# Performance work log

Measured on AMD Instinct MI355X. Metric: run time of the kernel, lower is better.

The kernel has to match this reference:

```python
import jax, jax.numpy as jnp
import numpy as np

N, M, RANK = 1024, 4096, 32


def setup_inputs() -> dict:
    key = jax.random.key(0)
    kW, kH, kT = jax.random.split(key, 3)
    W = jax.random.uniform(kW, (N, RANK), dtype=jnp.float32)
    H = jax.random.uniform(kH, (RANK, M), dtype=jnp.float32)
    tau = jax.random.uniform(kT, (N, RANK), dtype=jnp.float32) * 2.0 - 1.0
    return {"W": W, "H": H, "tau": tau}


def reference(W, H, tau):
    # Hf: FFT along last axis of softplus(H) -> (rank, M) complex64
    Hf = jnp.fft.fft(jax.nn.softplus(H), axis=-1)
    m = H.shape[-1]
    f = (jnp.arange(m, dtype=jnp.float32) / m)  # (M,)
    # phase ramp: omega[n,d,m] = exp(-i*2*pi*tau[n,d]*f[m])
    phase = tau[:, :, None] * f[None, None, :]          # (N, rank, M) float32
    omega = jnp.exp((-2j * jnp.pi) * phase)             # complex64
    spW = jax.nn.softplus(W)                            # (N, rank)
    # V[n,m] = sum_d spW[n,d] * omega[n,d,m] * Hf[d,m]
    V = jnp.einsum('nd,ndm,dm->nm', spW.astype(omega.dtype), omega, Hf)
    return V
```

## Files before the change

### kernel.cpp

```cpp
#include <hip/hip_runtime.h>
#include <hip/hip_bf16.h>
#include <math.h>

#ifndef M_PI
#define M_PI 3.14159265358979323846
#endif

constexpr int N    = 1024;
constexpr int M    = 4096;
constexpr int RANK = 32;
constexpr float PHI1 = -1.5339807878856412e-3f;

typedef __attribute__((ext_vector_type(8))) short bf16x8;
typedef __attribute__((ext_vector_type(4))) float f32x4;

__device__ __forceinline__ float softplus_f(float x) {
    const float t = __expf(-fabsf(x));
    return fmaxf(x, 0.0f) + __logf(1.0f + t);
}

__device__ __forceinline__ unsigned pack_bf16x2(float a, float b) {
    __hip_bfloat162 p;
    p.x = __float2bfloat16(a);
    p.y = __float2bfloat16(b);
    unsigned r;
    __builtin_memcpy(&r, &p, 4);
    return r;
}

__global__ __launch_bounds__(256) void dft_s1(const float* __restrict__ H,
                                              float* __restrict__ GR,
                                              float* __restrict__ GI) {
    __shared__ float sh[M];
    const int d = blockIdx.y, tid = threadIdx.x;
    const float4* H4 = (const float4*)(H + d * M);
    for (int i = tid; i < M / 4; i += 256) {
        const float4 v = H4[i];
        ((float4*)sh)[i] = make_float4(softplus_f(v.x), softplus_f(v.y),
                                       softplus_f(v.z), softplus_f(v.w));
    }
    __syncthreads();

    const int k0 = tid & 63;
    const int r0 = blockIdx.x * 8 + (tid >> 6) * 2;
    float twR0 = 1.f, twI0 = 0.f, aR0 = 0.f, aI0 = 0.f;
    float twR1 = 1.f, twI1 = 0.f, aR1 = 0.f, aI1 = 0.f;
    float s0, c0, s1, c1;
    __sincosf((-2.0f * (float)M_PI / 64.0f) * (float)r0,       &s0, &c0);
    __sincosf((-2.0f * (float)M_PI / 64.0f) * (float)(r0 + 1), &s1, &c1);

    for (int k1 = 0; k1 < 64; ++k1) {
        const float h = sh[(k1 << 6) + k0];
        aR0 = fmaf(h, twR0, aR0);  aI0 = fmaf(h, twI0, aI0);
        aR1 = fmaf(h, twR1, aR1);  aI1 = fmaf(h, twI1, aI1);
        float nR = fmaf(twR0, c0, -twI0 * s0);
        float nI = fmaf(twR0, s0,  twI0 * c0);
        twR0 = nR; twI0 = nI;
        nR = fmaf(twR1, c1, -twI1 * s1);
        nI = fmaf(twR1, s1,  twI1 * c1);
        twR1 = nR; twI1 = nI;
    }
    const int base = d * 4096 + r0 * 64 + k0;
    GR[base]      = aR0;  GI[base]      = aI0;
    GR[base + 64] = aR1;  GI[base + 64] = aI1;
}

__global__ __launch_bounds__(256) void dft_s2(const float* __restrict__ GR,
                                              const float* __restrict__ GI,
                                              float* __restrict__ HfR,
                                              float* __restrict__ HfI) {
    __shared__ float sGR[64 * 65], sGI[64 * 65];
    const int d = blockIdx.y, tid = threadIdx.x;
    const float4* gr4 = (const float4*)(GR + d * 4096);
    const float4* gi4 = (const float4*)(GI + d * 4096);
    for (int i4 = tid; i4 < 1024; i4 += 256) {
        const int r = i4 >> 4, k0 = (i4 & 15) << 2;
        const float4 vr = gr4[i4];
        const float4 vi = gi4[i4];
        const int p = r * 65 + k0;
        sGR[p] = vr.x; sGR[p+1] = vr.y; sGR[p+2] = vr.z; sGR[p+3] = vr.w;
        sGI[p] = vi.x; sGI[p+1] = vi.y; sGI[p+2] = vi.z; sGI[p+3] = vi.w;
    }
    __syncthreads();

    const int m = blockIdx.x * 256 + tid;
    const int rb = (m & 63) * 65;
    float ss, sc; __sincosf(PHI1 * (float)m, &ss, &sc);
    float tR_ = 1.f, tI_ = 0.f, accR = 0.f, accI = 0.f;
    #pragma unroll 8
    for (int k0 = 0; k0 < 64; ++k0) {
        const float gr = sGR[rb + k0], gi = sGI[rb + k0];
        accR = fmaf(tR_, gr, fmaf(-tI_, gi, accR));
        accI = fmaf(tR_, gi, fmaf( tI_, gr, accI));
        const float nR = fmaf(tR_, sc, -tI_ * ss);
        const float nI = fmaf(tR_, ss,  tI_ * sc);
        tR_ = nR; tI_ = nI;
    }
    HfR[d * M + m] = accR;
    HfI[d * M + m] = accI;
}

__device__ __forceinline__ void a_terms(float w, float t, float mcF, float* o) {
    const float sw = softplus_f(w);
    const float a1 = PHI1 * t;
    float s0, c0; __sincosf(a1 * mcF, &s0, &c0);
    const float R0 = sw * c0,  I0 = sw * s0;
    const float R1 = -a1 * I0, I1 = a1 * R0;
    const float h  = 0.5f * a1;
    const float R2 = -h * I1,  I2 = h * R1;
    o[0] = R0; o[1] = -I0; o[2] = R1; o[3] = -I1; o[4] = R2; o[5] = -I2;
}

__global__ __launch_bounds__(256, 4) void einsum_mfma(const float* __restrict__ W,
                                                      const float* __restrict__ tau,
                                                      const float* __restrict__ HfR,
                                                      const float* __restrict__ HfI,
                                                      float* __restrict__ out_f) {
    __shared__ __attribute__((aligned(16))) unsigned short sB[6][64][40];
    const int tid   = threadIdx.x;
    const int mBase = blockIdx.x * 64;
    const int nBase = blockIdx.y * 64;

    const int wv = tid >> 6, lane = tid & 63;
    const int q = lane >> 4, l = lane & 15;
    const int nA = nBase + wv * 16 + l;
    const int d8 = q << 3;
    const float mcF = (float)(mBase + 32);

    const float4 w0 = *(const float4*)(W   + nA * RANK + d8);
    const float4 w1 = *(const float4*)(W   + nA * RANK + d8 + 4);
    const float4 t0 = *(const float4*)(tau + nA * RANK + d8);
    const float4 t1 = *(const float4*)(tau + nA * RANK + d8 + 4);

    for (int e = tid; e < 512; e += 256) {
        const int mloc = e & 63;
        const int d0   = (e >> 6) << 2;
        const float dlt = (float)mloc - 32.0f;
        const float dq  = dlt * dlt;
        const float* pR = HfR + d0 * M + mBase + mloc;
        const float* pI = HfI + d0 * M + mBase + mloc;
        float r0 = pR[0], r1 = pR[M], r2 = pR[2*M], r3 = pR[3*M];
        float i0 = pI[0], i1 = pI[M], i2 = pI[2*M], i3 = pI[3*M];

        uint2 v;
        v.x = pack_bf16x2(r0, r1);           v.y = pack_bf16x2(r2, r3);
        *(uint2*)&sB[0][mloc][d0] = v;
        v.x = pack_bf16x2(i0, i1);           v.y = pack_bf16x2(i2, i3);
        *(uint2*)&sB[1][mloc][d0] = v;
        v.x = pack_bf16x2(r0*dlt, r1*dlt);   v.y = pack_bf16x2(r2*dlt, r3*dlt);
        *(uint2*)&sB[2][mloc][d0] = v;
        v.x = pack_bf16x2(i0*dlt, i1*dlt);   v.y = pack_bf16x2(i2*dlt, i3*dlt);
        *(uint2*)&sB[3][mloc][d0] = v;
        v.x = pack_bf16x2(r0*dq, r1*dq);     v.y = pack_bf16x2(r2*dq, r3*dq);
        *(uint2*)&sB[4][mloc][d0] = v;
        v.x = pack_bf16x2(i0*dq, i1*dq);     v.y = pack_bf16x2(i2*dq, i3*dq);
        *(uint2*)&sB[5][mloc][d0] = v;
    }

    const float wj[8] = {w0.x,w0.y,w0.z,w0.w,w1.x,w1.y,w1.z,w1.w};
    const float tj[8] = {t0.x,t0.y,t0.z,t0.w,t1.x,t1.y,t1.z,t1.w};
    unsigned uA[6][4];
    #pragma unroll
    for (int p = 0; p < 4; ++p) {
        float f0[6], f1[6];
        a_terms(wj[2*p],   tj[2*p],   mcF, f0);
        a_terms(wj[2*p+1], tj[2*p+1], mcF, f1);
        #pragma unroll
        for (int k = 0; k < 6; ++k) uA[k][p] = pack_bf16x2(f0[k], f1[k]);
    }
    bf16x8 fA[6];
    #pragma unroll
    for (int k = 0; k < 6; ++k) __builtin_memcpy(&fA[k], uA[k], 16);
    __syncthreads();

    for (int mt = 0; mt < 4; ++mt) {
        const int mL = (mt << 4) + l;
        const bf16x8 b0 = *(const bf16x8*)&sB[0][mL][d8];
        const bf16x8 b1 = *(const bf16x8*)&sB[1][mL][d8];
        const bf16x8 b2 = *(const bf16x8*)&sB[2][mL][d8];
        const bf16x8 b3 = *(const bf16x8*)&sB[3][mL][d8];
        const bf16x8 b4 = *(const bf16x8*)&sB[4][mL][d8];
        const bf16x8 b5 = *(const bf16x8*)&sB[5][mL][d8];

        f32x4 acc = {0.f, 0.f, 0.f, 0.f};
        acc = __builtin_amdgcn_mfma_f32_16x16x32_bf16(fA[0], b0, acc, 0, 0, 0);
        acc = __builtin_amdgcn_mfma_f32_16x16x32_bf16(fA[1], b1, acc, 0, 0, 0);
        acc = __builtin_amdgcn_mfma_f32_16x16x32_bf16(fA[2], b2, acc, 0, 0, 0);
        acc = __builtin_amdgcn_mfma_f32_16x16x32_bf16(fA[3], b3, acc, 0, 0, 0);
        acc = __builtin_amdgcn_mfma_f32_16x16x32_bf16(fA[4], b4, acc, 0, 0, 0);
        acc = __builtin_amdgcn_mfma_f32_16x16x32_bf16(fA[5], b5, acc, 0, 0, 0);

        #pragma unroll
        for (int r = 0; r < 4; ++r)
            out_f[(size_t)(nBase + wv * 16 + (q << 2) + r) * M
                  + mBase + (mt << 4) + l] = acc[r];
    }
}

__global__ __launch_bounds__(256) void dft_fused(const float* __restrict__ H,
                                                 float* __restrict__ HfR,
                                                 float* __restrict__ HfI) {
    __shared__ float  sh[M];
    __shared__ float2 sG[64 * 65];
    const int d = blockIdx.y, tid = threadIdx.x;
    for (int k = tid; k < M; k += 256) sh[k] = softplus_f(H[d * M + k]);
    __syncthreads();

    const int k0 = tid & 63;
    const int rB = (tid >> 6) * 16;
    float twR[16], twI[16], stR[16], stI[16], aR[16], aI[16];
    #pragma unroll
    for (int rr = 0; rr < 16; ++rr) {
        const float ang = (-2.0f * (float)M_PI / 64.0f) * (float)(rB + rr);
        __sincosf(ang, &stI[rr], &stR[rr]);
        twR[rr] = 1.f; twI[rr] = 0.f; aR[rr] = 0.f; aI[rr] = 0.f;
    }
    for (int k1 = 0; k1 < 64; ++k1) {
        const float h = sh[(k1 << 6) + k0];
        #pragma unroll
        for (int rr = 0; rr < 16; ++rr) {
            aR[rr] = fmaf(h, twR[rr], aR[rr]);
            aI[rr] = fmaf(h, twI[rr], aI[rr]);
            const float nR = fmaf(twR[rr], stR[rr], -twI[rr] * stI[rr]);
            const float nI = fmaf(twR[rr], stI[rr],  twI[rr] * stR[rr]);
            twR[rr] = nR; twI[rr] = nI;
        }
    }
    #pragma unroll
    for (int rr = 0; rr < 16; ++rr)
        sG[k0 * 65 + rB + rr] = make_float2(aR[rr], aI[rr]);
    __syncthreads();

    const int mBase = blockIdx.x * 1024;
    for (int j = 0; j < 4; ++j) {
        const int m = mBase + j * 256 + tid;
        const int r = m & 63;
        float ss, sc; __sincosf(PHI1 * (float)m, &ss, &sc);
        float tR_ = 1.f, tI_ = 0.f, accR = 0.f, accI = 0.f;
        #pragma unroll 8
        for (int qq = 0; qq < 64; ++qq) {
            const float2 g = sG[qq * 65 + r];
            accR = fmaf(tR_, g.x, fmaf(-tI_, g.y, accR));
            accI = fmaf(tR_, g.y, fmaf( tI_, g.x, accI));
            const float nR = fmaf(tR_, sc, -tI_ * ss);
            const float nI = fmaf(tR_, ss,  tI_ * sc);
            tR_ = nR; tI_ = nI;
        }
        HfR[d * M + m] = accR;
        HfI[d * M + m] = accI;
    }
}

template <bool CPLX, int U>
__global__ __launch_bounds__(256) void einsum_kernel(const float* __restrict__ W,
                                                     const float* __restrict__ tau,
                                                     const float* __restrict__ HfR,
                                                     const float* __restrict__ HfI,
                                                     float* __restrict__ out_f) {
    constexpr int ROWS = 16 * U;
    constexpr int MT   = 128;
    __shared__ float2 sHf[16 * MT];
    __shared__ float  sW[ROWS][RANK], sT[ROWS][RANK];
    const int tid   = threadIdx.x;
    const int mBase = blockIdx.x * MT;
    const int nBase = blockIdx.y * ROWS;

    for (int i = tid; i < ROWS * RANK; i += 256) {
        const int n_ = i >> 5, dd = i & 31;
        sW[n_][dd] = softplus_f(W[(nBase + n_) * RANK + dd]);
        sT[n_][dd] = tau[(nBase + n_) * RANK + dd];
    }

    const int nl = tid >> 4, chunk = tid & 15;
    const int m0 = mBase + (chunk << 3);

    float accR[U][8], accI[U][8];
    #pragma unroll
    for (int u = 0; u < U; ++u)
        #pragma unroll
        for (int j = 0; j < 8; ++j) { accR[u][j] = 0.f; if (CPLX) accI[u][j] = 0.f; }

    for (int half = 0; half < 2; ++half) {
        __syncthreads();
        for (int e = tid; e < 16 * 64; e += 256) {
            const int dl = e >> 6, p = e & 63;
            const int mm = p << 1;
            const int base = (half * 16 + dl) * M + mBase + mm;
            const float2 r2 = *(const float2*)(HfR + base);
            const float2 q2 = *(const float2*)(HfI + base);
            const int c = mm >> 3, j0 = mm & 7;
            float2* s2 = sHf + (dl << 7);
            s2[(j0 << 4) + c]       = make_float2(r2.x, q2.x);
            s2[((j0 + 1) << 4) + c] = make_float2(r2.y, q2.y);
        }
        __syncthreads();

        #pragma unroll 1
        for (int dl = 0; dl < 16; ++dl) {
            const int dd = (half << 4) + dl;
            float aR_[U], aI_[U], bR_[U], bI_[U], K[U];
            #pragma unroll
            for (int u = 0; u < U; ++u) {
                const float t = sT[nl * U + u][dd], w = sW[nl * U + u][dd];
                const float a1 = PHI1 * t;
                float sp, cp; __sincosf(a1, &sp, &cp);
                float s0, c0; __sincosf(a1 * (float)m0, &s0, &c0);
                aR_[u] = w * c0;
                aI_[u] = w * s0;
                bR_[u] = fmaf(aR_[u], cp, -aI_[u] * sp);
                bI_[u] = fmaf(aI_[u], cp,  aR_[u] * sp);
                K[u]   = 2.0f * cp;
            }
            int idx = (dl << 7) + chunk;
            #pragma unroll
            for (int j = 0; j < 8; ++j) {
                const float2 h = sHf[idx];
                #pragma unroll
                for (int u = 0; u < U; ++u) {
                    accR[u][j] = fmaf(aR_[u], h.x, fmaf(-aI_[u], h.y, accR[u][j]));
                    if (CPLX) accI[u][j] = fmaf(aR_[u], h.y, fmaf(aI_[u], h.x, accI[u][j]));
                    const float nR = fmaf(K[u], bR_[u], -aR_[u]);
                    const float nI = fmaf(K[u], bI_[u], -aI_[u]);
                    aR_[u] = bR_[u]; aI_[u] = bI_[u];
                    bR_[u] = nR;     bI_[u] = nI;
                }
                idx += 16;
            }
        }
    }

    #pragma unroll
    for (int u = 0; u < U; ++u) {
        const int n = nBase + nl * U + u;
        if (CPLX) {
            float2* o2 = ((float2*)out_f) + (size_t)n * M + m0;
            #pragma unroll
            for (int qq = 0; qq < 4; ++qq)
                ((float4*)o2)[qq] = make_float4(accR[u][2*qq], accI[u][2*qq],
                                                accR[u][2*qq+1], accI[u][2*qq+1]);
        } else {
            float* op = out_f + (size_t)n * M + m0;
            ((float4*)op)[0] = make_float4(accR[u][0], accR[u][1], accR[u][2], accR[u][3]);
            ((float4*)op)[1] = make_float4(accR[u][4], accR[u][5], accR[u][6], accR[u][7]);
        }
    }
}

__global__ __launch_bounds__(256) void tail_real(const float* __restrict__ W,
                                                 const float* __restrict__ tau,
                                                 const float* __restrict__ stashR,
                                                 const float* __restrict__ stashI,
                                                 float* __restrict__ out_f) {
    __shared__ float stR[32 * 32], stI[32 * 32];
    __shared__ float sW[64][RANK], sT[64][RANK];
    const int tid = threadIdx.x;
    const int c0  = blockIdx.x * 32;
    const int nBase = N - 64;
    for (int i = tid; i < 64 * RANK; i += 256) {
        const int n_ = i >> 5, dd = i & 31;
        sW[n_][dd] = softplus_f(W[(nBase + n_) * RANK + dd]);
        sT[n_][dd] = tau[(nBase + n_) * RANK + dd];
    }
    for (int i = tid; i < 32 * 32; i += 256) {
        const int d_ = i >> 5, mm = i & 31;
        stR[i] = stashR[d_ * M + c0 + mm];
        stI[i] = stashI[d_ * M + c0 + mm];
    }
    __syncthreads();
    const int n = tid >> 2, chunk = tid & 3;
    const int m0 = c0 + chunk;
    float acc[8];
    #pragma unroll
    for (int j = 0; j < 8; ++j) acc[j] = 0.f;
    for (int d = 0; d < RANK; ++d) {
        const float t = sT[n][d], w = sW[n][d];
        const float a1 = PHI1 * t;
        float ss, sc; __sincosf(a1 * 4.0f, &ss, &sc);
        float s0, c0f; __sincosf(a1 * (float)m0, &s0, &c0f);
        float tR_ = w * c0f, tI_ = w * s0;
        int idx = (d << 5) + chunk;
        #pragma unroll
        for (int j = 0; j < 8; ++j) {
            acc[j] = fmaf(tR_, stR[idx], fmaf(-tI_, stI[idx], acc[j]));
            const float nR = fmaf(tR_, sc, -tI_ * ss);
            const float nI = fmaf(tR_, ss,  tI_ * sc);
            tR_ = nR; tI_ = nI;
            idx += 4;
        }
    }
    #pragma unroll
    for (int j = 0; j < 8; ++j)
        out_f[(size_t)(nBase + n) * M + m0 + (j << 2)] = acc[j];
}

__global__ __launch_bounds__(256) void tail_cplx(const float* __restrict__ W,
                                                 const float* __restrict__ tau,
                                                 const float* __restrict__ stashR,
                                                 const float* __restrict__ stashI,
                                                 float* __restrict__ out_f) {
    const int nBase = N - 32;
    __shared__ float sW[32][RANK], sT[32][RANK];
    const int tid = threadIdx.x, mBase = blockIdx.x * 256;
    for (int i = tid; i < 32 * RANK; i += 256) {
        const int n_ = i >> 5, dd = i & 31;
        sW[n_][dd] = softplus_f(W[(nBase + n_) * RANK + dd]);
        sT[n_][dd] = tau[(nBase + n_) * RANK + dd];
    }
    const int m = mBase + tid;
    float hr[RANK], hi[RANK];
    #pragma unroll
    for (int d = 0; d < RANK; ++d) { hr[d] = stashR[d * M + m]; hi[d] = stashI[d * M + m]; }
    __syncthreads();
    const float phi = PHI1 * (float)m;
    for (int n_ = 0; n_ < 32; ++n_) {
        float aR = 0.f, aI = 0.f;
        #pragma unroll
        for (int d = 0; d < RANK; ++d) {
            const float t = sT[n_][d], w = sW[n_][d];
            float s, c; __sincosf(t * phi, &s, &c);
            const float cw = c * w, sw = s * w;
            aR = fmaf(cw, hr[d], fmaf(-sw, hi[d], aR));
            aI = fmaf(cw, hi[d], fmaf( sw, hr[d], aI));
        }
        ((float2*)out_f)[(size_t)(nBase + n_) * M + m] = make_float2(aR, aI);
    }
}

extern "C" void kernel_launch(void* const* d_in, const int* in_sizes, int n_in,
                              void* d_out, int out_size, void* d_ws, size_t ws_size,
                              hipStream_t stream) {
    const float* W   = (const float*)d_in[0];
    const float* H   = (const float*)d_in[1];
    const float* tau = (const float*)d_in[2];
    float* out_f = (float*)d_out;

    const bool   cplx   = (out_size >= 2 * N * M);
    const size_t planeN = (size_t)RANK * M;

    if (d_ws != nullptr && ws_size >= 4 * planeN * sizeof(float)) {
        float* HfR = (float*)d_ws;
        float* HfI = HfR + planeN;
        float* GR  = HfI + planeN;
        float* GI  = GR  + planeN;
        dft_s1<<<dim3(8, 32), 256, 0, stream>>>(H, GR, GI);
        dft_s2<<<dim3(16, 32), 256, 0, stream>>>(GR, GI, HfR, HfI);
        if (cplx)
            einsum_kernel<true , 2><<<dim3(32, N / 32), 256, 0, stream>>>(W, tau, HfR, HfI, out_f);
        else
            einsum_mfma<<<dim3(64, 16), 256, 0, stream>>>(W, tau, HfR, HfI, out_f);
    } else if (!cplx) {
        float* HfR = out_f + (size_t)(N - 64) * M;
        float* HfI = HfR + planeN;
        dft_fused<<<dim3(4, 32), 256, 0, stream>>>(H, HfR, HfI);
        einsum_kernel<false, 2><<<dim3(32, (N - 64) / 32), 256, 0, stream>>>(W, tau, HfR, HfI, out_f);
        tail_real<<<dim3(128), 256, 0, stream>>>(W, tau, HfR, HfI, out_f);
    } else {
        float* HfR = out_f + 2 * (size_t)N * M - 2 * planeN;
        float* HfI = HfR + planeN;
        dft_fused<<<dim3(4, 32), 256, 0, stream>>>(H, HfR, HfI);
        einsum_kernel<true , 2><<<dim3(32, (N - 32) / 32), 256, 0, stream>>>(W, tau, HfR, HfI, out_f);
        tail_cplx<<<dim3(16), 256, 0, stream>>>(W, tau, HfR, HfI, out_f);
    }
}
```

Before: 82.09 us.

## Fuse DFT stages and MFMA einsum into one cooperative kernel with grid syncs

Replaces the three separate launches (two DFT stages and the MFMA einsum) on the real-output path with a single cooperative kernel of 1024 blocks that separates the phases with grid-wide syncs. The aim is to remove kernel launch gaps and inter-kernel tail effects. The cost is that only 512 blocks work during the DFT phases, and each grid sync adds its own overhead. If the cooperative launch fails, the code falls back to the old three-kernel path.

```diff
diff --git a/kernel.cpp b/kernel.cpp
--- a/kernel.cpp
+++ b/kernel.cpp
@@ -1,10 +1,13 @@
 #include <hip/hip_runtime.h>
+#include <hip/hip_cooperative_groups.h>
 #include <hip/hip_bf16.h>
 #include <math.h>
 
 #ifndef M_PI
 #define M_PI 3.14159265358979323846
 #endif
+
+namespace cg = cooperative_groups;
 
 constexpr int N    = 1024;
 constexpr int M    = 4096;
@@ -26,6 +29,174 @@
     unsigned r;
     __builtin_memcpy(&r, &p, 4);
     return r;
+}
+
+__device__ __forceinline__ void a_terms(float w, float t, float mcF, float* o) {
+    const float sw = softplus_f(w);
+    const float a1 = PHI1 * t;
+    float s0, c0; __sincosf(a1 * mcF, &s0, &c0);
+    const float R0 = sw * c0,  I0 = sw * s0;
+    const float R1 = -a1 * I0, I1 = a1 * R0;
+    const float h  = 0.5f * a1;
+    const float R2 = -h * I1,  I2 = h * R1;
+    o[0] = R0; o[1] = -I0; o[2] = R1; o[3] = -I1; o[4] = R2; o[5] = -I2;
+}
+
+__global__ __launch_bounds__(256, 4) void mega_real(const float* __restrict__ W,
+                                                    const float* __restrict__ tau,
+                                                    const float* __restrict__ H,
+                                                    float* __restrict__ GR,
+                                                    float* __restrict__ GI,
+                                                    float* __restrict__ HfR,
+                                                    float* __restrict__ HfI,
+                                                    float* __restrict__ out_f) {
+    __shared__ __attribute__((aligned(16))) char smem[64 * 65 * 8];
+    const int tid = threadIdx.x;
+    const int bx  = blockIdx.x;
+    cg::grid_group grid = cg::this_grid();
+
+    if (bx < 512) {
+        float* sh = (float*)smem;
+        const int d  = bx >> 4;
+        const int rG = bx & 15;
+        const float4* H4 = (const float4*)(H + d * M);
+        for (int i = tid; i < M / 4; i += 256) {
+            const float4 v = H4[i];
+            ((float4*)sh)[i] = make_float4(softplus_f(v.x), softplus_f(v.y),
+                                           softplus_f(v.z), softplus_f(v.w));
+        }
+        __syncthreads();
+        const int k0 = tid & 63;
+        const int r0 = rG * 4 + (tid >> 6);
+        float s0, c0;
+        __sincosf((-2.0f * (float)M_PI / 64.0f) * (float)r0, &s0, &c0);
+        float twR = 1.f, twI = 0.f, aR = 0.f, aI = 0.f;
+        for (int k1 = 0; k1 < 64; ++k1) {
+            const float h = sh[(k1 << 6) + k0];
+            aR = fmaf(h, twR, aR);  aI = fmaf(h, twI, aI);
+            const float nR = fmaf(twR, c0, -twI * s0);
+            const float nI = fmaf(twR, s0,  twI * c0);
+            twR = nR; twI = nI;
+        }
+        const int base = d * 4096 + r0 * 64 + k0;
+        GR[base] = aR;  GI[base] = aI;
+    }
+    __threadfence();
+    grid.sync();
+
+    if (bx < 512) {
+        float* sGR = (float*)smem;
+        float* sGI = sGR + 64 * 65;
+        const int d  = bx >> 4;
+        const int mG = bx & 15;
+        const float4* gr4 = (const float4*)(GR + d * 4096);
+        const float4* gi4 = (const float4*)(GI + d * 4096);
+        for (int i4 = tid; i4 < 1024; i4 += 256) {
+            const int r = i4 >> 4, k0 = (i4 & 15) << 2;
+            const float4 vr = gr4[i4];
+            const float4 vi = gi4[i4];
+            const int p = r * 65 + k0;
+            sGR[p] = vr.x; sGR[p+1] = vr.y; sGR[p+2] = vr.z; sGR[p+3] = vr.w;
+            sGI[p] = vi.x; sGI[p+1] = vi.y; sGI[p+2] = vi.z; sGI[p+3] = vi.w;
+        }
+        __syncthreads();
+        const int m  = mG * 256 + tid;
+        const int rb = (m & 63) * 65;
+        float ss, sc; __sincosf(PHI1 * (float)m, &ss, &sc);
+        float tR_ = 1.f, tI_ = 0.f, accR = 0.f, accI = 0.f;
+        #pragma unroll 8
+        for (int k0 = 0; k0 < 64; ++k0) {
+            const float gr = sGR[rb + k0], gi = sGI[rb + k0];
+            accR = fmaf(tR_, gr, fmaf(-tI_, gi, accR));
+            accI = fmaf(tR_, gi, fmaf( tI_, gr, accI));
+            const float nR = fmaf(tR_, sc, -tI_ * ss);
+            const float nI = fmaf(tR_, ss,  tI_ * sc);
+            tR_ = nR; tI_ = nI;
+        }
+        HfR[d * M + m] = accR;
+        HfI[d * M + m] = accI;
+    }
+    __threadfence();
+    grid.sync();
+
+    typedef unsigned short (*sBp_t)[64][40];
+    sBp_t sB = (sBp_t)smem;
+    const int mBase = (bx & 63) << 6;
+    const int nBase = (bx >> 6) << 6;
+    const int wv = tid >> 6, lane = tid & 63;
+    const int q = lane >> 4, l = lane & 15;
+    const int nA = nBase + wv * 16 + l;
+    const int d8 = q << 3;
+    const float mcF = (float)(mBase + 32);
+
+    const float4 w0 = *(const float4*)(W   + nA * RANK + d8);
+    const float4 w1 = *(const float4*)(W   + nA * RANK + d8 + 4);
+    const float4 t0 = *(const float4*)(tau + nA * RANK + d8);
+    const float4 t1 = *(const float4*)(tau + nA * RANK + d8 + 4);
+
+    for (int e = tid; e < 512; e += 256) {
+        const int mloc = e & 63;
+        const int d0   = (e >> 6) << 2;
+        const float dlt = (float)mloc - 32.0f;
+        const float dq  = dlt * dlt;
+        const float* pR = HfR + d0 * M + mBase + mloc;
+        const float* pI = HfI + d0 * M + mBase + mloc;
+        float r0 = pR[0], r1 = pR[M], r2 = pR[2*M], r3 = pR[3*M];
+        float i0 = pI[0], i1 = pI[M], i2 = pI[2*M], i3 = pI[3*M];
+
+        uint2 v;
+        v.x = pack_bf16x2(r0, r1);           v.y = pack_bf16x2(r2, r3);
+        *(uint2*)&sB[0][mloc][d0] = v;
+        v.x = pack_bf16x2(i0, i1);           v.y = pack_bf16x2(i2, i3);
+        *(uint2*)&sB[1][mloc][d0] = v;
+        v.x = pack_bf16x2(r0*dlt, r1*dlt);   v.y = pack_bf16x2(r2*dlt, r3*dlt);
+        *(uint2*)&sB[2][mloc][d0] = v;
+        v.x = pack_bf16x2(i0*dlt, i1*dlt);   v.y = pack_bf16x2(i2*dlt, i3*dlt);
+        *(uint2*)&sB[3][mloc][d0] = v;
+        v.x = pack_bf16x2(r0*dq, r1*dq);     v.y = pack_bf16x2(r2*dq, r3*dq);
+        *(uint2*)&sB[4][mloc][d0] = v;
+        v.x = pack_bf16x2(i0*dq, i1*dq);     v.y = pack_bf16x2(i2*dq, i3*dq);
+        *(uint2*)&sB[5][mloc][d0] = v;
+    }
+
+    const float wj[8] = {w0.x,w0.y,w0.z,w0.w,w1.x,w1.y,w1.z,w1.w};
+    const float tj[8] = {t0.x,t0.y,t0.z,t0.w,t1.x,t1.y,t1.z,t1.w};
+    unsigned uA[6][4];
+    #pragma unroll
+    for (int p = 0; p < 4; ++p) {
+        float f0[6], f1[6];
+        a_terms(wj[2*p],   tj[2*p],   mcF, f0);
+        a_terms(wj[2*p+1], tj[2*p+1], mcF, f1);
+        #pragma unroll
+        for (int k = 0; k < 6; ++k) uA[k][p] = pack_bf16x2(f0[k], f1[k]);
+    }
+    bf16x8 fA[6];
+    #pragma unroll
+    for (int k = 0; k < 6; ++k) __builtin_memcpy(&fA[k], uA[k], 16);
+    __syncthreads();
+
+    for (int mt = 0; mt < 4; ++mt) {
+        const int mL = (mt << 4) + l;
+        const bf16x8 b0 = *(const bf16x8*)&sB[0][mL][d8];
+        const bf16x8 b1 = *(const bf16x8*)&sB[1][mL][d8];
+        const bf16x8 b2 = *(const bf16x8*)&sB[2][mL][d8];
+        const bf16x8 b3 = *(const bf16x8*)&sB[3][mL][d8];
+        const bf16x8 b4 = *(const bf16x8*)&sB[4][mL][d8];
+        const bf16x8 b5 = *(const bf16x8*)&sB[5][mL][d8];
+
+        f32x4 acc = {0.f, 0.f, 0.f, 0.f};
+        acc = __builtin_amdgcn_mfma_f32_16x16x32_bf16(fA[0], b0, acc, 0, 0, 0);
+        acc = __builtin_amdgcn_mfma_f32_16x16x32_bf16(fA[1], b1, acc, 0, 0, 0);
+        acc = __builtin_amdgcn_mfma_f32_16x16x32_bf16(fA[2], b2, acc, 0, 0, 0);
+        acc = __builtin_amdgcn_mfma_f32_16x16x32_bf16(fA[3], b3, acc, 0, 0, 0);
+        acc = __builtin_amdgcn_mfma_f32_16x16x32_bf16(fA[4], b4, acc, 0, 0, 0);
+        acc = __builtin_amdgcn_mfma_f32_16x16x32_bf16(fA[5], b5, acc, 0, 0, 0);
+
+        #pragma unroll
+        for (int r = 0; r < 4; ++r)
+            out_f[(size_t)(nBase + wv * 16 + (q << 2) + r) * M
+                  + mBase + (mt << 4) + l] = acc[r];
+    }
 }
 
 __global__ __launch_bounds__(256) void dft_s1(const float* __restrict__ H,
@@ -98,17 +269,6 @@
     }
     HfR[d * M + m] = accR;
     HfI[d * M + m] = accI;
-}
-
-__device__ __forceinline__ void a_terms(float w, float t, float mcF, float* o) {
-    const float sw = softplus_f(w);
-    const float a1 = PHI1 * t;
-    float s0, c0; __sincosf(a1 * mcF, &s0, &c0);
-    const float R0 = sw * c0,  I0 = sw * s0;
-    const float R1 = -a1 * I0, I1 = a1 * R0;
-    const float h  = 0.5f * a1;
-    const float R2 = -h * I1,  I2 = h * R1;
-    o[0] = R0; o[1] = -I0; o[2] = R1; o[3] = -I1; o[4] = R2; o[5] = -I2;
 }
 
 __global__ __launch_bounds__(256, 4) void einsum_mfma(const float* __restrict__ W,
@@ -437,17 +597,34 @@
     const bool   cplx   = (out_size >= 2 * N * M);
     const size_t planeN = (size_t)RANK * M;
 
+    static int coop_ok = -1;
+
     if (d_ws != nullptr && ws_size >= 4 * planeN * sizeof(float)) {
         float* HfR = (float*)d_ws;
         float* HfI = HfR + planeN;
         float* GR  = HfI + planeN;
         float* GI  = GR  + planeN;
-        dft_s1<<<dim3(8, 32), 256, 0, stream>>>(H, GR, GI);
-        dft_s2<<<dim3(16, 32), 256, 0, stream>>>(GR, GI, HfR, HfI);
-        if (cplx)
+
+        if (!cplx) {
+            if (coop_ok != 0) {
+                void* args[8] = {(void*)&W, (void*)&tau, (void*)&H,
+                                 (void*)&GR, (void*)&GI,
+                                 (void*)&HfR, (void*)&HfI, (void*)&out_f};
+                const hipError_t e = hipLaunchCooperativeKernel(
+                    reinterpret_cast<const void*>(mega_real),
+                    dim3(1024), dim3(256), args, 0u, stream);
+                if (e == hipSuccess) { coop_ok = 1; return; }
+                coop_ok = 0;
+                (void)hipGetLastError();
+            }
+            dft_s1<<<dim3(8, 32), 256, 0, stream>>>(H, GR, GI);
+            dft_s2<<<dim3(16, 32), 256, 0, stream>>>(GR, GI, HfR, HfI);
+            einsum_mfma<<<dim3(64, 16), 256, 0, stream>>>(W, tau, HfR, HfI, out_f);
+        } else {
+            dft_s1<<<dim3(8, 32), 256, 0, stream>>>(H, GR, GI);
+            dft_s2<<<dim3(16, 32), 256, 0, stream>>>(GR, GI, HfR, HfI);
             einsum_kernel<true , 2><<<dim3(32, N / 32), 256, 0, stream>>>(W, tau, HfR, HfI, out_f);
-        else
-            einsum_mfma<<<dim3(64, 16), 256, 0, stream>>>(W, tau, HfR, HfI, out_f);
+        }
     } else if (!cplx) {
         float* HfR = out_f + (size_t)(N - 64) * M;
         float* HfI = HfR + planeN;
```

New measurement: 81.58 us. About the same (-0.6%).

## Fuse two-stage DFT into one kernel with residue-class block decomposition

Applied to the files above, without the earlier changes.

Replaces the two DFT kernels, which passed intermediate G arrays through global memory, with one kernel. Each block handles one residue class c of the output frequency modulo 8, computes the 8 first-stage rows it needs into shared memory, then produces the 512 outputs with m ≡ c mod 8. This removes the global round trip for the intermediates and one kernel launch. In exchange, every block recomputes softplus over the full H row (8x redundant loads and softplus work), and the second-stage shared reads come from rows indexed by tid&7, so lanes in a warp read different rows.

```diff
diff --git a/kernel.cpp b/kernel.cpp
--- a/kernel.cpp
+++ b/kernel.cpp
@@ -26,78 +26,6 @@
     unsigned r;
     __builtin_memcpy(&r, &p, 4);
     return r;
-}
-
-__global__ __launch_bounds__(256) void dft_s1(const float* __restrict__ H,
-                                              float* __restrict__ GR,
-                                              float* __restrict__ GI) {
-    __shared__ float sh[M];
-    const int d = blockIdx.y, tid = threadIdx.x;
-    const float4* H4 = (const float4*)(H + d * M);
-    for (int i = tid; i < M / 4; i += 256) {
-        const float4 v = H4[i];
-        ((float4*)sh)[i] = make_float4(softplus_f(v.x), softplus_f(v.y),
-                                       softplus_f(v.z), softplus_f(v.w));
-    }
-    __syncthreads();
-
-    const int k0 = tid & 63;
-    const int r0 = blockIdx.x * 8 + (tid >> 6) * 2;
-    float twR0 = 1.f, twI0 = 0.f, aR0 = 0.f, aI0 = 0.f;
-    float twR1 = 1.f, twI1 = 0.f, aR1 = 0.f, aI1 = 0.f;
-    float s0, c0, s1, c1;
-    __sincosf((-2.0f * (float)M_PI / 64.0f) * (float)r0,       &s0, &c0);
-    __sincosf((-2.0f * (float)M_PI / 64.0f) * (float)(r0 + 1), &s1, &c1);
-
-    for (int k1 = 0; k1 < 64; ++k1) {
-        const float h = sh[(k1 << 6) + k0];
-        aR0 = fmaf(h, twR0, aR0);  aI0 = fmaf(h, twI0, aI0);
-        aR1 = fmaf(h, twR1, aR1);  aI1 = fmaf(h, twI1, aI1);
-        float nR = fmaf(twR0, c0, -twI0 * s0);
-        float nI = fmaf(twR0, s0,  twI0 * c0);
-        twR0 = nR; twI0 = nI;
-        nR = fmaf(twR1, c1, -twI1 * s1);
-        nI = fmaf(twR1, s1,  twI1 * c1);
-        twR1 = nR; twI1 = nI;
-    }
-    const int base = d * 4096 + r0 * 64 + k0;
-    GR[base]      = aR0;  GI[base]      = aI0;
-    GR[base + 64] = aR1;  GI[base + 64] = aI1;
-}
-
-__global__ __launch_bounds__(256) void dft_s2(const float* __restrict__ GR,
-                                              const float* __restrict__ GI,
-                                              float* __restrict__ HfR,
-                                              float* __restrict__ HfI) {
-    __shared__ float sGR[64 * 65], sGI[64 * 65];
-    const int d = blockIdx.y, tid = threadIdx.x;
-    const float4* gr4 = (const float4*)(GR + d * 4096);
-    const float4* gi4 = (const float4*)(GI + d * 4096);
-    for (int i4 = tid; i4 < 1024; i4 += 256) {
-        const int r = i4 >> 4, k0 = (i4 & 15) << 2;
-        const float4 vr = gr4[i4];
-        const float4 vi = gi4[i4];
-        const int p = r * 65 + k0;
-        sGR[p] = vr.x; sGR[p+1] = vr.y; sGR[p+2] = vr.z; sGR[p+3] = vr.w;
-        sGI[p] = vi.x; sGI[p+1] = vi.y; sGI[p+2] = vi.z; sGI[p+3] = vi.w;
-    }
-    __syncthreads();
-
-    const int m = blockIdx.x * 256 + tid;
-    const int rb = (m & 63) * 65;
-    float ss, sc; __sincosf(PHI1 * (float)m, &ss, &sc);
-    float tR_ = 1.f, tI_ = 0.f, accR = 0.f, accI = 0.f;
-    #pragma unroll 8
-    for (int k0 = 0; k0 < 64; ++k0) {
-        const float gr = sGR[rb + k0], gi = sGI[rb + k0];
-        accR = fmaf(tR_, gr, fmaf(-tI_, gi, accR));
-        accI = fmaf(tR_, gi, fmaf( tI_, gr, accI));
-        const float nR = fmaf(tR_, sc, -tI_ * ss);
-        const float nI = fmaf(tR_, ss,  tI_ * sc);
-        tR_ = nR; tI_ = nI;
-    }
-    HfR[d * M + m] = accR;
-    HfI[d * M + m] = accI;
 }
 
 __device__ __forceinline__ void a_terms(float w, float t, float mcF, float* o) {
@@ -109,6 +37,70 @@
     const float h  = 0.5f * a1;
     const float R2 = -h * I1,  I2 = h * R1;
     o[0] = R0; o[1] = -I0; o[2] = R1; o[3] = -I1; o[4] = R2; o[5] = -I2;
+}
+
+__global__ __launch_bounds__(256) void dft_bal(const float* __restrict__ H,
+                                               float* __restrict__ HfR,
+                                               float* __restrict__ HfI) {
+    __shared__ float  sh[M];
+    __shared__ float2 sG[8 * 65];
+    const int c   = blockIdx.x;
+    const int d   = blockIdx.y;
+    const int tid = threadIdx.x;
+
+    const float4* H4 = (const float4*)(H + d * M);
+    for (int i = tid; i < M / 4; i += 256) {
+        const float4 v = H4[i];
+        ((float4*)sh)[i] = make_float4(softplus_f(v.x), softplus_f(v.y),
+                                       softplus_f(v.z), softplus_f(v.w));
+    }
+    __syncthreads();
+
+    {
+        const int k0   = tid & 63;
+        const int rgrp = tid >> 6;
+        const int rr0  = rgrp * 2;
+        const int r0   = c + 8 * rr0;
+        const int r1   = r0 + 8;
+        float s0, c0, s1, c1;
+        __sincosf((-2.0f * (float)M_PI / 64.0f) * (float)r0, &s0, &c0);
+        __sincosf((-2.0f * (float)M_PI / 64.0f) * (float)r1, &s1, &c1);
+        float twR0 = 1.f, twI0 = 0.f, aR0 = 0.f, aI0 = 0.f;
+        float twR1 = 1.f, twI1 = 0.f, aR1 = 0.f, aI1 = 0.f;
+        for (int k1 = 0; k1 < 64; ++k1) {
+            const float h = sh[(k1 << 6) + k0];
+            aR0 = fmaf(h, twR0, aR0);  aI0 = fmaf(h, twI0, aI0);
+            aR1 = fmaf(h, twR1, aR1);  aI1 = fmaf(h, twI1, aI1);
+            float nR = fmaf(twR0, c0, -twI0 * s0);
+            float nI = fmaf(twR0, s0,  twI0 * c0);
+            twR0 = nR; twI0 = nI;
+            nR = fmaf(twR1, c1, -twI1 * s1);
+            nI = fmaf(twR1, s1,  twI1 * c1);
+            twR1 = nR; twI1 = nI;
+        }
+        sG[rr0 * 65 + k0]       = make_float2(aR0, aI0);
+        sG[(rr0 + 1) * 65 + k0] = make_float2(aR1, aI1);
+    }
+    __syncthreads();
+
+    const int rr = tid & 7;
+    #pragma unroll
+    for (int j = 0; j < 2; ++j) {
+        const int m = c + 8 * (tid + 256 * j);
+        float ss, sc; __sincosf(PHI1 * (float)m, &ss, &sc);
+        float tR_ = 1.f, tI_ = 0.f, accR = 0.f, accI = 0.f;
+        #pragma unroll 8
+        for (int k0 = 0; k0 < 64; ++k0) {
+            const float2 g = sG[rr * 65 + k0];
+            accR = fmaf(tR_, g.x, fmaf(-tI_, g.y, accR));
+            accI = fmaf(tR_, g.y, fmaf( tI_, g.x, accI));
+            const float nR = fmaf(tR_, sc, -tI_ * ss);
+            const float nI = fmaf(tR_, ss,  tI_ * sc);
+            tR_ = nR; tI_ = nI;
+        }
+        HfR[d * M + m] = accR;
+        HfI[d * M + m] = accI;
+    }
 }
 
 __global__ __launch_bounds__(256, 4) void einsum_mfma(const float* __restrict__ W,
@@ -440,10 +432,7 @@
     if (d_ws != nullptr && ws_size >= 4 * planeN * sizeof(float)) {
         float* HfR = (float*)d_ws;
         float* HfI = HfR + planeN;
-        float* GR  = HfI + planeN;
-        float* GI  = GR  + planeN;
-        dft_s1<<<dim3(8, 32), 256, 0, stream>>>(H, GR, GI);
-        dft_s2<<<dim3(16, 32), 256, 0, stream>>>(GR, GI, HfR, HfI);
+        dft_bal<<<dim3(8, 32), 256, 0, stream>>>(H, HfR, HfI);
         if (cplx)
             einsum_kernel<true , 2><<<dim3(32, N / 32), 256, 0, stream>>>(W, tau, HfR, HfI, out_f);
         else
```

New measurement: 78.34 us. -4.6%, faster.
